# Optimization experiments

Hardware: AMD Instinct MI355X
Metric: run time of the kernel (lower is better)

Reference implementation:

```python
import jax, jax.numpy as jnp
import numpy as np

B = 262144          # batch of sample points
L = 16              # hash levels
T = 1 << 19         # hash table size per level
F = 2               # features per level
BASE_RES = 16
FINEST_RES = 512
DH = 64             # density MLP hidden
DOUT = 16           # density MLP out (density_out dim)
CH = 64             # color MLP hidden
PRIMES = np.array([1, 2654435761, 805459861], dtype=np.uint32)
_b = np.exp((np.log(FINEST_RES) - np.log(BASE_RES)) / (L - 1))
RES = jnp.asarray(np.floor(BASE_RES * _b ** np.arange(L)).astype(np.float32))  # (L,)


def _linear_init(key, fan_in, fan_out):
    kw, kb = jax.random.split(key)
    bound = 1.0 / np.sqrt(fan_in)
    w = jax.random.uniform(kw, (fan_in, fan_out), minval=-bound, maxval=bound)
    b = jax.random.uniform(kb, (fan_out,), minval=-bound, maxval=bound)
    return w, b


def setup_inputs() -> dict:
    key = jax.random.key(0)
    ks = jax.random.split(key, 10)
    coords = jax.random.uniform(ks[0], (B, 3), dtype=jnp.float32)          # in [0,1]
    directions = jax.random.normal(ks[1], (B, 3), dtype=jnp.float32)
    embeddings = jax.random.uniform(ks[2], (L, T, F), minval=-1e-4, maxval=1e-4, dtype=jnp.float32)
    dw1, db1 = _linear_init(ks[3], L * F, DH)
    dw2, db2 = _linear_init(ks[4], DH, DOUT)
    cw1, cb1 = _linear_init(ks[5], 16 + DOUT, CH)
    cw2, cb2 = _linear_init(ks[6], CH, CH)
    cw3, cb3 = _linear_init(ks[7], CH, CH)
    cw4, cb4 = _linear_init(ks[8], CH, 3)
    return dict(coords=coords, directions=directions, embeddings=embeddings,
                dw1=dw1, db1=db1, dw2=dw2, db2=db2,
                cw1=cw1, cb1=cb1, cw2=cw2, cb2=cb2,
                cw3=cw3, cb3=cb3, cw4=cw4, cb4=cb4)


def hash_encode(coords, embeddings):
    # coords: (B,3) in [0,1]; embeddings: (L,T,F)
    pos = coords[:, None, :] * RES[None, :, None]            # (B,L,3)
    p0 = jnp.floor(pos)
    frac = pos - p0                                           # (B,L,3)
    p0 = p0.astype(jnp.uint32)
    corners = jnp.stack([p0, p0 + jnp.uint32(1)], axis=-1)    # (B,L,3,2)
    h_ax = corners * jnp.asarray(PRIMES)[None, None, :, None]  # uint32 wraparound
    hidx = (h_ax[:, :, 0, :, None, None]
            ^ h_ax[:, :, 1, None, :, None]
            ^ h_ax[:, :, 2, None, None, :])                   # (B,L,2,2,2)
    hidx = (hidx & jnp.uint32(T - 1)).reshape(coords.shape[0], L, 8).astype(jnp.int32)
    feats = embeddings[jnp.arange(L)[None, :, None], hidx]    # (B,L,8,F)
    wx = jnp.stack([1.0 - frac[..., 0], frac[..., 0]], -1)    # (B,L,2)
    wy = jnp.stack([1.0 - frac[..., 1], frac[..., 1]], -1)
    wz = jnp.stack([1.0 - frac[..., 2], frac[..., 2]], -1)
    w = (wx[:, :, :, None, None] * wy[:, :, None, :, None] * wz[:, :, None, None, :])
    w = w.reshape(coords.shape[0], L, 8)                      # (B,L,8)
    out = jnp.sum(feats * w[..., None], axis=2)               # (B,L,F)
    return out.reshape(coords.shape[0], L * F)


def sh_encode_deg4(d):
    # d: (B,3) unit directions in [-1,1]; degree-4 real SH basis (16 comps)
    x, y, z = d[:, 0], d[:, 1], d[:, 2]
    xx, yy, zz = x * x, y * y, z * z
    xy, yz, xz = x * y, y * z, x * z
    c = jnp.full_like(x, 0.28209479177387814)
    return jnp.stack([
        c,
        -0.48860251190291987 * y,
        0.48860251190291987 * z,
        -0.48860251190291987 * x,
        1.0925484305920792 * xy,
        -1.0925484305920792 * yz,
        0.94617469575755997 * zz - 0.31539156525251999,
        -1.0925484305920792 * xz,
        0.54627421529603959 * (xx - yy),
        0.59004358992664352 * y * (-3.0 * xx + yy),
        2.8906114426405538 * xy * z,
        0.45704579946446572 * y * (1.0 - 5.0 * zz),
        0.3731763325901154 * z * (5.0 * zz - 3.0),
        0.45704579946446572 * x * (1.0 - 5.0 * zz),
        1.4453057213202769 * z * (xx - yy),
        0.59004358992664352 * x * (xx - 3.0 * yy),
    ], axis=1)


def reference(coords, directions, embeddings, dw1, db1, dw2, db2,
              cw1, cb1, cw2, cb2, cw3, cb3, cw4, cb4):
    # density net: hash encode -> Linear+ReLU -> Linear
    feat = hash_encode(coords, embeddings)                    # (B, L*F)
    h = jax.nn.relu(feat @ dw1 + db1)
    density_out = h @ dw2 + db2                               # (B, DOUT)
    density = jnp.exp(density_out[:, 0])                      # TruncExp fwd = exp
    # color net
    d = directions / jnp.linalg.norm(directions, axis=1, keepdims=True)
    d01 = (d + 1.0) / 2.0                                     # remap as in module
    sh = sh_encode_deg4(d01 * 2.0 - 1.0)                      # encoder maps back to [-1,1]
    inp = jnp.concatenate([sh, density_out], axis=1)          # (B, 32)
    x = jax.nn.relu(inp @ cw1 + cb1)
    x = jax.nn.relu(x @ cw2 + cb2)
    x = jax.nn.relu(x @ cw3 + cb3)
    color = jax.nn.sigmoid(x @ cw4 + cb4)                     # (B, 3)
    return density, color
```

## Files before the change

### kernel.cpp

```cpp
#include <hip/hip_runtime.h>
#include <cmath>

#define NPTS 262144
#define NLVL 16
#define TBL  524288u
#define TMASK 524287u
#define TPB  128
#define NQ   7

typedef __attribute__((ext_vector_type(8))) short short8;
typedef __attribute__((ext_vector_type(4))) float f32x4;

struct ResArr { float r[NLVL]; };
struct QuadInfo { int off[NQ]; int dim[NQ]; };

__device__ __forceinline__ unsigned short f2bf(float f) {
    union { float f; unsigned u; } v; v.f = f;
    unsigned r = v.u + 0x7FFFu + ((v.u >> 16) & 1u);
    return (unsigned short)(r >> 16);
}
__device__ __forceinline__ float blo(unsigned u) {
    union { unsigned v; float f; } x; x.v = u << 16; return x.f;
}
__device__ __forceinline__ float bhi(unsigned u) {
    union { unsigned v; float f; } x; x.v = u & 0xffff0000u; return x.f;
}

#define MFMA(a,b,c) __builtin_amdgcn_mfma_f32_16x16x32_bf16((a),(b),(c),0,0,0)

__global__ __launch_bounds__(256) void wpack_k(
    const float* __restrict__ dw1, const float* __restrict__ db1,
    const float* __restrict__ dw2, const float* __restrict__ db2,
    const float* __restrict__ cw1, const float* __restrict__ cb1,
    const float* __restrict__ cw2, const float* __restrict__ cb2,
    const float* __restrict__ cw3, const float* __restrict__ cb3,
    const float* __restrict__ cw4, const float* __restrict__ cb4,
    unsigned short* __restrict__ wpk, float* __restrict__ bpk)
{
    const int tid  = threadIdx.x;
    const int wid  = tid >> 6;
    const int lane = tid & 63;
    const int m16  = lane & 15;
    const int q    = lane >> 4;

    const unsigned char MAT[28] = {0,0,0,0, 1,1, 2,2,2,2, 3,3,3,3,3,3,3,3, 4,4,4,4,4,4,4,4, 5,5};
    const unsigned char K0 [28] = {0,0,0,0, 0,32, 0,0,0,0, 0,0,0,0,32,32,32,32, 0,0,0,0,32,32,32,32, 0,32};
    const unsigned char N0 [28] = {0,16,32,48, 0,0, 0,16,32,48, 0,16,32,48,0,16,32,48, 0,16,32,48,0,16,32,48, 0,0};

    #pragma unroll
    for (int s = 0; s < 28; ++s) {
        if ((s & 3) == wid) {
            const int mat = MAT[s];
            const float* src = mat==0?dw1 : mat==1?dw2 : mat==2?cw1 : mat==3?cw2 : mat==4?cw3 : cw4;
            const int fan = (mat==1) ? 16 : (mat==5) ? 3 : 64;
            const int k = (int)K0[s] + q*8;
            const int n = (int)N0[s] + m16;
            unsigned short u[8];
            #pragma unroll
            for (int j = 0; j < 8; ++j) {
                float v = 0.f;
                if (mat != 5 || n < 3) v = src[(k+j)*fan + n];
                u[j] = f2bf(v);
            }
            unsigned* w32 = (unsigned*)(wpk + s*512 + lane*8);
            w32[0] = (unsigned)u[0] | ((unsigned)u[1] << 16);
            w32[1] = (unsigned)u[2] | ((unsigned)u[3] << 16);
            w32[2] = (unsigned)u[4] | ((unsigned)u[5] << 16);
            w32[3] = (unsigned)u[6] | ((unsigned)u[7] << 16);
        }
    }
    {
        int t = tid;
        if      (t <  64) bpk[t] = db1[t];
        else if (t <  80) bpk[t] = db2[t-64];
        else if (t < 144) bpk[t] = cb1[t-80];
        else if (t < 208) bpk[t] = cb2[t-144];
    }
    if (tid < 80) {
        int t = tid + 208;
        if (t < 272) bpk[t] = cb3[t-208];
        else         bpk[t] = (t-272 < 3) ? cb4[t-272] : 0.f;
    }
}

__global__ __launch_bounds__(256) void densify_quad_k(
    const float* __restrict__ emb,
    uint4* __restrict__ quad,
    QuadInfo qi)
{
    const int l = blockIdx.y;
    const int t = blockIdx.x * 256 + threadIdx.x;
    const int D = qi.dim[l];
    if (t >= D*D*D) return;
    const unsigned z = (unsigned)t % (unsigned)D;
    const unsigned rem = (unsigned)t / (unsigned)D;
    const unsigned y = rem % (unsigned)D;
    const unsigned x = rem / (unsigned)D;

    const float2* __restrict__ emb2 = (const float2*)emb;
    const unsigned base = (unsigned)l * TBL;
    const unsigned hy0 = y*2654435761u, hy1 = (y+1u)*2654435761u;
    const unsigned hz0 = z*805459861u,  hz1 = (z+1u)*805459861u;

    const float2 a = emb2[base + ((x^hy0^hz0)&TMASK)];
    const float2 b = emb2[base + ((x^hy0^hz1)&TMASK)];
    const float2 c = emb2[base + ((x^hy1^hz0)&TMASK)];
    const float2 d = emb2[base + ((x^hy1^hz1)&TMASK)];

    uint4 q;
    q.x = (unsigned)f2bf(a.x) | ((unsigned)f2bf(a.y) << 16);
    q.y = (unsigned)f2bf(b.x) | ((unsigned)f2bf(b.y) << 16);
    q.z = (unsigned)f2bf(c.x) | ((unsigned)f2bf(c.y) << 16);
    q.w = (unsigned)f2bf(d.x) | ((unsigned)f2bf(d.y) << 16);
    quad[qi.off[l] + t] = q;
}

__global__ __launch_bounds__(256) void hash_encode_k(
    const float* __restrict__ coords,
    const float* __restrict__ emb,
    const uint4* __restrict__ quad,
    unsigned* __restrict__ featws,
    ResArr res, QuadInfo qi)
{
    const int tid = threadIdx.x;
    const int b   = blockIdx.x;
    const int xcd = b & 7;
    const int s   = b >> 3;

    if (s < 1152) {
        int l, p;
        if (s < 1024) {
            l = 7 + xcd;
            p = s * 256 + tid;
        } else {
            l = 15;
            p = xcd * 32768 + (s - 1024) * 256 + tid;
        }

        const float cx = coords[3*p], cy = coords[3*p+1], cz = coords[3*p+2];
        const float r = res.r[l];
        const float px = cx*r, py = cy*r, pz = cz*r;
        const float fpx = floorf(px), fpy = floorf(py), fpz = floorf(pz);
        const float fx = px-fpx, fy = py-fpy, fz = pz-fpz;
        const unsigned ix=(unsigned)fpx, iy=(unsigned)fpy, iz=(unsigned)fpz;
        const unsigned hx0=ix,             hx1=ix+1u;
        const unsigned hy0=iy*2654435761u, hy1=(iy+1u)*2654435761u;
        const unsigned hz0=iz*805459861u,  hz1=(iz+1u)*805459861u;
        const unsigned base = (unsigned)l * TBL;
        const float2* __restrict__ emb2 = (const float2*)emb;

        const float2 f000 = emb2[base + ((hx0^hy0^hz0)&TMASK)];
        const float2 f001 = emb2[base + ((hx0^hy0^hz1)&TMASK)];
        const float2 f010 = emb2[base + ((hx0^hy1^hz0)&TMASK)];
        const float2 f011 = emb2[base + ((hx0^hy1^hz1)&TMASK)];
        const float2 f100 = emb2[base + ((hx1^hy0^hz0)&TMASK)];
        const float2 f101 = emb2[base + ((hx1^hy0^hz1)&TMASK)];
        const float2 f110 = emb2[base + ((hx1^hy1^hz0)&TMASK)];
        const float2 f111 = emb2[base + ((hx1^hy1^hz1)&TMASK)];

        const float wx0=1.f-fx, wy0=1.f-fy, wz0=1.f-fz;
        float o0, o1;
        o0 = wx0*wy0*wz0*f000.x;                 o1 = wx0*wy0*wz0*f000.y;
        o0 = fmaf(wx0*wy0*fz,  f001.x, o0);      o1 = fmaf(wx0*wy0*fz,  f001.y, o1);
        o0 = fmaf(wx0*fy*wz0,  f010.x, o0);      o1 = fmaf(wx0*fy*wz0,  f010.y, o1);
        o0 = fmaf(wx0*fy*fz,   f011.x, o0);      o1 = fmaf(wx0*fy*fz,   f011.y, o1);
        o0 = fmaf(fx*wy0*wz0,  f100.x, o0);      o1 = fmaf(fx*wy0*wz0,  f100.y, o1);
        o0 = fmaf(fx*wy0*fz,   f101.x, o0);      o1 = fmaf(fx*wy0*fz,   f101.y, o1);
        o0 = fmaf(fx*fy*wz0,   f110.x, o0);      o1 = fmaf(fx*fy*wz0,   f110.y, o1);
        o0 = fmaf(fx*fy*fz,    f111.x, o0);      o1 = fmaf(fx*fy*fz,    f111.y, o1);

        featws[(size_t)l * NPTS + p] = (unsigned)f2bf(o0) | ((unsigned)f2bf(o1) << 16);
    } else {
        const int g  = xcd * 224 + (s - 1152);
        const int l  = g >> 8;
        const int c  = g & 255;
        const int D  = qi.dim[l];
        const int DD = D*D;
        const int off = qi.off[l];
        const float r = res.r[l];

        int   pidx[4];
        uint4 qA[4], qB[4];
        float fxa[4], fya[4], fza[4];
        #pragma unroll
        for (int k = 0; k < 4; ++k) {
            const int p = c*1024 + k*256 + tid;
            pidx[k] = p;
            const float cx = coords[3*p], cy = coords[3*p+1], cz = coords[3*p+2];
            const float px = cx*r, py = cy*r, pz = cz*r;
            const float fpx = floorf(px), fpy = floorf(py), fpz = floorf(pz);
            fxa[k] = px-fpx; fya[k] = py-fpy; fza[k] = pz-fpz;
            const int ix=(int)fpx, iy=(int)fpy, iz=(int)fpz;
            const int v0 = off + (ix*D + iy)*D + iz;
            qA[k] = quad[v0];
            qB[k] = quad[v0 + DD];
        }
        #pragma unroll
        for (int k = 0; k < 4; ++k) {
            const float fx = fxa[k], fy = fya[k], fz = fza[k];
            const float wx0=1.f-fx, wy0=1.f-fy, wz0=1.f-fz;
            const float w000=wx0*wy0*wz0, w001=wx0*wy0*fz;
            const float w010=wx0*fy*wz0,  w011=wx0*fy*fz;
            const float w100=fx*wy0*wz0,  w101=fx*wy0*fz;
            const float w110=fx*fy*wz0,   w111=fx*fy*fz;
            float o0, o1;
            o0 = w000*blo(qA[k].x);              o1 = w000*bhi(qA[k].x);
            o0 = fmaf(w001, blo(qA[k].y), o0);   o1 = fmaf(w001, bhi(qA[k].y), o1);
            o0 = fmaf(w010, blo(qA[k].z), o0);   o1 = fmaf(w010, bhi(qA[k].z), o1);
            o0 = fmaf(w011, blo(qA[k].w), o0);   o1 = fmaf(w011, bhi(qA[k].w), o1);
            o0 = fmaf(w100, blo(qB[k].x), o0);   o1 = fmaf(w100, bhi(qB[k].x), o1);
            o0 = fmaf(w101, blo(qB[k].y), o0);   o1 = fmaf(w101, bhi(qB[k].y), o1);
            o0 = fmaf(w110, blo(qB[k].z), o0);   o1 = fmaf(w110, bhi(qB[k].z), o1);
            o0 = fmaf(w111, blo(qB[k].w), o0);   o1 = fmaf(w111, bhi(qB[k].w), o1);
            featws[(size_t)l * NPTS + pidx[k]] =
                (unsigned)f2bf(o0) | ((unsigned)f2bf(o1) << 16);
        }
    }
}

__global__ __launch_bounds__(256, 3) void mlp_mfma_k(
    const unsigned* __restrict__ featws,
    const unsigned short* __restrict__ wpk,
    const float* __restrict__ bpk,
    const float* __restrict__ dirs,
    float* __restrict__ out)
{
    const int tid  = threadIdx.x;
    const int wid  = tid >> 6;
    const int lane = tid & 63;
    const int m16  = lane & 15;
    const int q    = lane >> 4;

    __shared__ __align__(16) unsigned short wlds[28 * 512];
    __shared__ float blds[288];
    __shared__ __align__(16) unsigned short featL[TPB * 40];
    __shared__ __align__(16) unsigned short actL[4 * 16 * 72];

    {
        uint4* dst = (uint4*)wlds;
        const uint4* srcv = (const uint4*)wpk;
        #pragma unroll
        for (int j = 0; j < 7; ++j) dst[j*256 + tid] = srcv[j*256 + tid];
        if (tid < 288) blds[tid] = bpk[tid];
        if (tid < 32)  blds[256 + tid] = bpk[256 + tid];
    }

    const int pbase = blockIdx.x * TPB;
    unsigned* fL32 = (unsigned*)featL;
    #pragma unroll
    for (int j = 0; j < 8; ++j) {
        const int idx  = j*256 + tid;
        const int l    = idx >> 7;
        const int ploc = idx & 127;
        fL32[ploc*20 + l] = featws[(size_t)l * NPTS + pbase + ploc];
    }
    __syncthreads();

    unsigned short* aw = actL + wid*1152;
    const short8* wfr = (const short8*)wlds;

    #pragma unroll
    for (int iter = 0; iter < 2; ++iter) {
        const int tile = wid + 4*iter;
        const int loc0 = tile*16;
        const int p0g  = pbase + loc0;

        short8 a0 = *(const short8*)(featL + (loc0+m16)*40 + q*8);
        f32x4 acc[4];
        #pragma unroll
        for (int nc = 0; nc < 4; ++nc) {
            const float b = blds[nc*16 + m16];
            acc[nc] = (f32x4){b,b,b,b};
            acc[nc] = MFMA(a0, wfr[nc*64 + lane], acc[nc]);
        }
        #pragma unroll
        for (int nc = 0; nc < 4; ++nc)
            #pragma unroll
            for (int r = 0; r < 4; ++r)
                aw[(q*4+r)*72 + nc*16 + m16] = f2bf(fmaxf(acc[nc][r], 0.f));

        short8 ad0 = *(const short8*)(aw + m16*72 + q*8);
        short8 ad1 = *(const short8*)(aw + m16*72 + 32 + q*8);
        f32x4 dob;
        { const float b = blds[64 + m16]; dob = (f32x4){b,b,b,b}; }
        dob = MFMA(ad0, wfr[4*64 + lane], dob);
        dob = MFMA(ad1, wfr[5*64 + lane], dob);

        if (m16 == 0) {
            #pragma unroll
            for (int r = 0; r < 4; ++r) out[p0g + q*4 + r] = expf(dob[r]);
        }

        #pragma unroll
        for (int r = 0; r < 4; ++r)
            aw[(q*4+r)*72 + 16 + m16] = f2bf(dob[r]);
        {
            const int pg = p0g + m16;
            const float dx0 = dirs[3*pg], dy0 = dirs[3*pg+1], dz0 = dirs[3*pg+2];
            const float inv = 1.f / sqrtf(dx0*dx0 + dy0*dy0 + dz0*dz0);
            float x = dx0*inv, y = dy0*inv, z = dz0*inv;
            x = ((x+1.f)*0.5f)*2.f - 1.f;
            y = ((y+1.f)*0.5f)*2.f - 1.f;
            z = ((z+1.f)*0.5f)*2.f - 1.f;
            float s0, s1, s2, s3;
            switch (q) {
            case 0: s0 = 0.28209479177387814f;
                    s1 = -0.48860251190291987f*y;
                    s2 =  0.48860251190291987f*z;
                    s3 = -0.48860251190291987f*x; break;
            case 1: s0 =  1.0925484305920792f*x*y;
                    s1 = -1.0925484305920792f*y*z;
                    s2 =  0.94617469575756f*z*z - 0.31539156525252f;
                    s3 = -1.0925484305920792f*x*z; break;
            case 2: s0 =  0.5462742152960396f*(x*x - y*y);
                    s1 =  0.5900435899266435f*y*(-3.f*x*x + y*y);
                    s2 =  2.890611442640554f*x*y*z;
                    s3 =  0.4570457994644657f*y*(1.f - 5.f*z*z); break;
            default:s0 =  0.3731763325901154f*z*(5.f*z*z - 3.f);
                    s1 =  0.4570457994644657f*x*(1.f - 5.f*z*z);
                    s2 =  1.445305721320277f*z*(x*x - y*y);
                    s3 =  0.5900435899266435f*x*(x*x - 3.f*y*y); break;
            }
            unsigned* ip = (unsigned*)(aw + m16*72 + q*4);
            ip[0] = (unsigned)f2bf(s0) | ((unsigned)f2bf(s1) << 16);
            ip[1] = (unsigned)f2bf(s2) | ((unsigned)f2bf(s3) << 16);
        }

        short8 ac0 = *(const short8*)(aw + m16*72 + q*8);
        #pragma unroll
        for (int nc = 0; nc < 4; ++nc) {
            const float b = blds[80 + nc*16 + m16];
            acc[nc] = (f32x4){b,b,b,b};
            acc[nc] = MFMA(ac0, wfr[(6+nc)*64 + lane], acc[nc]);
        }
        #pragma unroll
        for (int nc = 0; nc < 4; ++nc)
            #pragma unroll
            for (int r = 0; r < 4; ++r)
                aw[(q*4+r)*72 + nc*16 + m16] = f2bf(fmaxf(acc[nc][r], 0.f));

        short8 a20 = *(const short8*)(aw + m16*72 + q*8);
        short8 a21 = *(const short8*)(aw + m16*72 + 32 + q*8);
        #pragma unroll
        for (int nc = 0; nc < 4; ++nc) {
            const float b = blds[144 + nc*16 + m16];
            acc[nc] = (f32x4){b,b,b,b};
            acc[nc] = MFMA(a20, wfr[(10+nc)*64 + lane], acc[nc]);
            acc[nc] = MFMA(a21, wfr[(14+nc)*64 + lane], acc[nc]);
        }
        #pragma unroll
        for (int nc = 0; nc < 4; ++nc)
            #pragma unroll
            for (int r = 0; r < 4; ++r)
                aw[(q*4+r)*72 + nc*16 + m16] = f2bf(fmaxf(acc[nc][r], 0.f));

        short8 a30 = *(const short8*)(aw + m16*72 + q*8);
        short8 a31 = *(const short8*)(aw + m16*72 + 32 + q*8);
        #pragma unroll
        for (int nc = 0; nc < 4; ++nc) {
            const float b = blds[208 + nc*16 + m16];
            acc[nc] = (f32x4){b,b,b,b};
            acc[nc] = MFMA(a30, wfr[(18+nc)*64 + lane], acc[nc]);
            acc[nc] = MFMA(a31, wfr[(22+nc)*64 + lane], acc[nc]);
        }
        #pragma unroll
        for (int nc = 0; nc < 4; ++nc)
            #pragma unroll
            for (int r = 0; r < 4; ++r)
                aw[(q*4+r)*72 + nc*16 + m16] = f2bf(fmaxf(acc[nc][r], 0.f));

        short8 a40 = *(const short8*)(aw + m16*72 + q*8);
        short8 a41 = *(const short8*)(aw + m16*72 + 32 + q*8);
        f32x4 c4;
        { const float b = blds[272 + m16]; c4 = (f32x4){b,b,b,b}; }
        c4 = MFMA(a40, wfr[26*64 + lane], c4);
        c4 = MFMA(a41, wfr[27*64 + lane], c4);
        if (m16 < 3) {
            #pragma unroll
            for (int r = 0; r < 4; ++r)
                out[NPTS + 3*(p0g + q*4 + r) + m16] = 1.f / (1.f + expf(-c4[r]));
        }
    }
}

extern "C" void kernel_launch(void* const* d_in, const int* in_sizes, int n_in,
                              void* d_out, int out_size, void* d_ws, size_t ws_size,
                              hipStream_t stream)
{
    ResArr res;
    const double b = exp((log(512.0) - log(16.0)) / 15.0);
    for (int l = 0; l < NLVL; ++l)
        res.r[l] = (float)floor(16.0 * pow(b, (double)l));

    QuadInfo qi;
    int off = 0, maxn = 0;
    for (int l = 0; l < NQ; ++l) {
        const int D = (int)res.r[l] + 1;
        qi.dim[l] = D;
        qi.off[l] = off;
        off += D*D*D;
        if (D*D*D > maxn) maxn = D*D*D;
    }

    unsigned*       featws = (unsigned*)d_ws;
    uint4*          quad   = (uint4*)((char*)d_ws + (size_t)NLVL * NPTS * 4);
    unsigned short* wpk    = (unsigned short*)((char*)quad + (size_t)off * 16);
    float*          bpk    = (float*)((char*)wpk + 28 * 512 * 2);

    wpack_k<<<1, 256, 0, stream>>>(
        (const float*)d_in[3],  (const float*)d_in[4],
        (const float*)d_in[5],  (const float*)d_in[6],
        (const float*)d_in[7],  (const float*)d_in[8],
        (const float*)d_in[9],  (const float*)d_in[10],
        (const float*)d_in[11], (const float*)d_in[12],
        (const float*)d_in[13], (const float*)d_in[14],
        wpk, bpk);

    densify_quad_k<<<dim3((maxn + 255)/256, NQ), 256, 0, stream>>>(
        (const float*)d_in[2], quad, qi);

    hash_encode_k<<<11008, 256, 0, stream>>>(
        (const float*)d_in[0],
        (const float*)d_in[2],
        quad, featws, res, qi);

    mlp_mfma_k<<<NPTS/TPB, 256, 0, stream>>>(
        featws, wpk, bpk,
        (const float*)d_in[1],
        (float*)d_out);
}
```

Baseline: 254.6 us.

## Store interleaved octet corner data for coarse levels and fuse prep kernels

The densified table for levels 0-5 now stores all eight corners of each cell as two adjacent uint4 entries. A lookup therefore reads 32 contiguous bytes instead of two uint4 loads a full D*D slab apart. Level 6 keeps the old quad layout. The weight-packing kernel and the densify kernel are merged into one launch to drop one kernel launch, at the cost of doubling the dense table storage and densify gather work for the coarse levels.

Result: no change. 259.2 us (+1.8%).

```diff
diff --git a/kernel.cpp b/kernel.cpp
--- a/kernel.cpp
+++ b/kernel.cpp
@@ -25,10 +25,15 @@
 __device__ __forceinline__ float bhi(unsigned u) {
     union { unsigned v; float f; } x; x.v = u & 0xffff0000u; return x.f;
 }
+__device__ __forceinline__ unsigned packbf(float a, float b) {
+    return (unsigned)f2bf(a) | ((unsigned)f2bf(b) << 16);
+}
 
 #define MFMA(a,b,c) __builtin_amdgcn_mfma_f32_16x16x32_bf16((a),(b),(c),0,0,0)
 
-__global__ __launch_bounds__(256) void wpack_k(
+__global__ __launch_bounds__(256) void prep_k(
+    const float* __restrict__ emb,
+    uint4* __restrict__ octq, QuadInfo qi,
     const float* __restrict__ dw1, const float* __restrict__ db1,
     const float* __restrict__ dw2, const float* __restrict__ db2,
     const float* __restrict__ cw1, const float* __restrict__ cb1,
@@ -37,59 +42,56 @@
     const float* __restrict__ cw4, const float* __restrict__ cb4,
     unsigned short* __restrict__ wpk, float* __restrict__ bpk)
 {
-    const int tid  = threadIdx.x;
-    const int wid  = tid >> 6;
-    const int lane = tid & 63;
-    const int m16  = lane & 15;
-    const int q    = lane >> 4;
-
-    const unsigned char MAT[28] = {0,0,0,0, 1,1, 2,2,2,2, 3,3,3,3,3,3,3,3, 4,4,4,4,4,4,4,4, 5,5};
-    const unsigned char K0 [28] = {0,0,0,0, 0,32, 0,0,0,0, 0,0,0,0,32,32,32,32, 0,0,0,0,32,32,32,32, 0,32};
-    const unsigned char N0 [28] = {0,16,32,48, 0,0, 0,16,32,48, 0,16,32,48,0,16,32,48, 0,16,32,48,0,16,32,48, 0,0};
-
-    #pragma unroll
-    for (int s = 0; s < 28; ++s) {
-        if ((s & 3) == wid) {
-            const int mat = MAT[s];
-            const float* src = mat==0?dw1 : mat==1?dw2 : mat==2?cw1 : mat==3?cw2 : mat==4?cw3 : cw4;
-            const int fan = (mat==1) ? 16 : (mat==5) ? 3 : 64;
-            const int k = (int)K0[s] + q*8;
-            const int n = (int)N0[s] + m16;
-            unsigned short u[8];
-            #pragma unroll
-            for (int j = 0; j < 8; ++j) {
-                float v = 0.f;
-                if (mat != 5 || n < 3) v = src[(k+j)*fan + n];
-                u[j] = f2bf(v);
+    const int l = blockIdx.y;
+    const int tid = threadIdx.x;
+
+    if (l == 7) {
+        if (blockIdx.x != 0) return;
+        const int wid  = tid >> 6;
+        const int lane = tid & 63;
+        const int m16  = lane & 15;
+        const int q    = lane >> 4;
+        const unsigned char MAT[28] = {0,0,0,0, 1,1, 2,2,2,2, 3,3,3,3,3,3,3,3, 4,4,4,4,4,4,4,4, 5,5};
+        const unsigned char K0 [28] = {0,0,0,0, 0,32, 0,0,0,0, 0,0,0,0,32,32,32,32, 0,0,0,0,32,32,32,32, 0,32};
+        const unsigned char N0 [28] = {0,16,32,48, 0,0, 0,16,32,48, 0,16,32,48,0,16,32,48, 0,16,32,48,0,16,32,48, 0,0};
+        #pragma unroll
+        for (int s = 0; s < 28; ++s) {
+            if ((s & 3) == wid) {
+                const int mat = MAT[s];
+                const float* src = mat==0?dw1 : mat==1?dw2 : mat==2?cw1 : mat==3?cw2 : mat==4?cw3 : cw4;
+                const int fan = (mat==1) ? 16 : (mat==5) ? 3 : 64;
+                const int k = (int)K0[s] + q*8;
+                const int n = (int)N0[s] + m16;
+                unsigned short u[8];
+                #pragma unroll
+                for (int j = 0; j < 8; ++j) {
+                    float v = 0.f;
+                    if (mat != 5 || n < 3) v = src[(k+j)*fan + n];
+                    u[j] = f2bf(v);
+                }
+                unsigned* w32 = (unsigned*)(wpk + s*512 + lane*8);
+                w32[0] = (unsigned)u[0] | ((unsigned)u[1] << 16);
+                w32[1] = (unsigned)u[2] | ((unsigned)u[3] << 16);
+                w32[2] = (unsigned)u[4] | ((unsigned)u[5] << 16);
+                w32[3] = (unsigned)u[6] | ((unsigned)u[7] << 16);
             }
-            unsigned* w32 = (unsigned*)(wpk + s*512 + lane*8);
-            w32[0] = (unsigned)u[0] | ((unsigned)u[1] << 16);
-            w32[1] = (unsigned)u[2] | ((unsigned)u[3] << 16);
-            w32[2] = (unsigned)u[4] | ((unsigned)u[5] << 16);
-            w32[3] = (unsigned)u[6] | ((unsigned)u[7] << 16);
-        }
-    }
-    {
-        int t = tid;
-        if      (t <  64) bpk[t] = db1[t];
-        else if (t <  80) bpk[t] = db2[t-64];
-        else if (t < 144) bpk[t] = cb1[t-80];
-        else if (t < 208) bpk[t] = cb2[t-144];
-    }
-    if (tid < 80) {
-        int t = tid + 208;
-        if (t < 272) bpk[t] = cb3[t-208];
-        else         bpk[t] = (t-272 < 3) ? cb4[t-272] : 0.f;
-    }
-}
-
-__global__ __launch_bounds__(256) void densify_quad_k(
-    const float* __restrict__ emb,
-    uint4* __restrict__ quad,
-    QuadInfo qi)
-{
-    const int l = blockIdx.y;
-    const int t = blockIdx.x * 256 + threadIdx.x;
+        }
+        {
+            int t = tid;
+            if      (t <  64) bpk[t] = db1[t];
+            else if (t <  80) bpk[t] = db2[t-64];
+            else if (t < 144) bpk[t] = cb1[t-80];
+            else if (t < 208) bpk[t] = cb2[t-144];
+        }
+        if (tid < 80) {
+            int t = tid + 208;
+            if (t < 272) bpk[t] = cb3[t-208];
+            else         bpk[t] = (t-272 < 3) ? cb4[t-272] : 0.f;
+        }
+        return;
+    }
+
+    const int t = blockIdx.x * 256 + tid;
     const int D = qi.dim[l];
     if (t >= D*D*D) return;
     const unsigned z = (unsigned)t % (unsigned)D;
@@ -102,23 +104,38 @@
     const unsigned hy0 = y*2654435761u, hy1 = (y+1u)*2654435761u;
     const unsigned hz0 = z*805459861u,  hz1 = (z+1u)*805459861u;
 
-    const float2 a = emb2[base + ((x^hy0^hz0)&TMASK)];
-    const float2 b = emb2[base + ((x^hy0^hz1)&TMASK)];
-    const float2 c = emb2[base + ((x^hy1^hz0)&TMASK)];
-    const float2 d = emb2[base + ((x^hy1^hz1)&TMASK)];
-
-    uint4 q;
-    q.x = (unsigned)f2bf(a.x) | ((unsigned)f2bf(a.y) << 16);
-    q.y = (unsigned)f2bf(b.x) | ((unsigned)f2bf(b.y) << 16);
-    q.z = (unsigned)f2bf(c.x) | ((unsigned)f2bf(c.y) << 16);
-    q.w = (unsigned)f2bf(d.x) | ((unsigned)f2bf(d.y) << 16);
-    quad[qi.off[l] + t] = q;
+    const float2 a0 = emb2[base + ((x^hy0^hz0)&TMASK)];
+    const float2 b0 = emb2[base + ((x^hy0^hz1)&TMASK)];
+    const float2 c0 = emb2[base + ((x^hy1^hz0)&TMASK)];
+    const float2 d0 = emb2[base + ((x^hy1^hz1)&TMASK)];
+    uint4 qa;
+    qa.x = packbf(a0.x, a0.y);
+    qa.y = packbf(b0.x, b0.y);
+    qa.z = packbf(c0.x, c0.y);
+    qa.w = packbf(d0.x, d0.y);
+
+    if (l < 6) {
+        const unsigned x1 = x + 1u;
+        const float2 a1 = emb2[base + ((x1^hy0^hz0)&TMASK)];
+        const float2 b1 = emb2[base + ((x1^hy0^hz1)&TMASK)];
+        const float2 c1 = emb2[base + ((x1^hy1^hz0)&TMASK)];
+        const float2 d1 = emb2[base + ((x1^hy1^hz1)&TMASK)];
+        uint4 qb;
+        qb.x = packbf(a1.x, a1.y);
+        qb.y = packbf(b1.x, b1.y);
+        qb.z = packbf(c1.x, c1.y);
+        qb.w = packbf(d1.x, d1.y);
+        octq[qi.off[l] + 2*t]     = qa;
+        octq[qi.off[l] + 2*t + 1] = qb;
+    } else {
+        octq[qi.off[6] + t] = qa;
+    }
 }
 
 __global__ __launch_bounds__(256) void hash_encode_k(
     const float* __restrict__ coords,
     const float* __restrict__ emb,
-    const uint4* __restrict__ quad,
+    const uint4* __restrict__ octq,
     unsigned* __restrict__ featws,
     ResArr res, QuadInfo qi)
 {
@@ -169,7 +186,7 @@
         o0 = fmaf(fx*fy*wz0,   f110.x, o0);      o1 = fmaf(fx*fy*wz0,   f110.y, o1);
         o0 = fmaf(fx*fy*fz,    f111.x, o0);      o1 = fmaf(fx*fy*fz,    f111.y, o1);
 
-        featws[(size_t)l * NPTS + p] = (unsigned)f2bf(o0) | ((unsigned)f2bf(o1) << 16);
+        featws[(size_t)l * NPTS + p] = packbf(o0, o1);
     } else {
         const int g  = xcd * 224 + (s - 1152);
         const int l  = g >> 8;
@@ -191,9 +208,14 @@
             const float fpx = floorf(px), fpy = floorf(py), fpz = floorf(pz);
             fxa[k] = px-fpx; fya[k] = py-fpy; fza[k] = pz-fpz;
             const int ix=(int)fpx, iy=(int)fpy, iz=(int)fpz;
-            const int v0 = off + (ix*D + iy)*D + iz;
-            qA[k] = quad[v0];
-            qB[k] = quad[v0 + DD];
+            const int v0 = (ix*D + iy)*D + iz;
+            if (l < 6) {
+                qA[k] = octq[off + 2*v0];
+                qB[k] = octq[off + 2*v0 + 1];
+            } else {
+                qA[k] = octq[off + v0];
+                qB[k] = octq[off + v0 + DD];
+            }
         }
         #pragma unroll
         for (int k = 0; k < 4; ++k) {
@@ -212,8 +234,7 @@
             o0 = fmaf(w101, blo(qB[k].y), o0);   o1 = fmaf(w101, bhi(qB[k].y), o1);
             o0 = fmaf(w110, blo(qB[k].z), o0);   o1 = fmaf(w110, bhi(qB[k].z), o1);
             o0 = fmaf(w111, blo(qB[k].w), o0);   o1 = fmaf(w111, bhi(qB[k].w), o1);
-            featws[(size_t)l * NPTS + pidx[k]] =
-                (unsigned)f2bf(o0) | ((unsigned)f2bf(o1) << 16);
+            featws[(size_t)l * NPTS + pidx[k]] = packbf(o0, o1);
         }
     }
 }
@@ -241,7 +262,7 @@
         const uint4* srcv = (const uint4*)wpk;
         #pragma unroll
         for (int j = 0; j < 7; ++j) dst[j*256 + tid] = srcv[j*256 + tid];
-        if (tid < 288) blds[tid] = bpk[tid];
+        if (tid < 256) blds[tid] = bpk[tid];
         if (tid < 32)  blds[256 + tid] = bpk[256 + tid];
     }
 
@@ -322,8 +343,8 @@
                     s3 =  0.5900435899266435f*x*(x*x - 3.f*y*y); break;
             }
             unsigned* ip = (unsigned*)(aw + m16*72 + q*4);
-            ip[0] = (unsigned)f2bf(s0) | ((unsigned)f2bf(s1) << 16);
-            ip[1] = (unsigned)f2bf(s2) | ((unsigned)f2bf(s3) << 16);
+            ip[0] = packbf(s0, s1);
+            ip[1] = packbf(s2, s3);
         }
 
         short8 ac0 = *(const short8*)(aw + m16*72 + q*8);
@@ -398,16 +419,18 @@
         const int D = (int)res.r[l] + 1;
         qi.dim[l] = D;
         qi.off[l] = off;
-        off += D*D*D;
-        if (D*D*D > maxn) maxn = D*D*D;
+        const int n = D*D*D;
+        off += (l < 6) ? 2*n : n;
+        if (n > maxn) maxn = n;
     }
 
     unsigned*       featws = (unsigned*)d_ws;
-    uint4*          quad   = (uint4*)((char*)d_ws + (size_t)NLVL * NPTS * 4);
-    unsigned short* wpk    = (unsigned short*)((char*)quad + (size_t)off * 16);
+    uint4*          octq   = (uint4*)((char*)d_ws + (size_t)NLVL * NPTS * 4);
+    unsigned short* wpk    = (unsigned short*)((char*)octq + (size_t)off * 16);
     float*          bpk    = (float*)((char*)wpk + 28 * 512 * 2);
 
-    wpack_k<<<1, 256, 0, stream>>>(
+    prep_k<<<dim3((maxn + 255)/256, 8), 256, 0, stream>>>(
+        (const float*)d_in[2], octq, qi,
         (const float*)d_in[3],  (const float*)d_in[4],
         (const float*)d_in[5],  (const float*)d_in[6],
         (const float*)d_in[7],  (const float*)d_in[8],
@@ -416,13 +439,10 @@
         (const float*)d_in[13], (const float*)d_in[14],
         wpk, bpk);
 
-    densify_quad_k<<<dim3((maxn + 255)/256, NQ), 256, 0, stream>>>(
-        (const float*)d_in[2], quad, qi);
-
     hash_encode_k<<<11008, 256, 0, stream>>>(
         (const float*)d_in[0],
         (const float*)d_in[2],
-        quad, featws, res, qi);
+        octq, featws, res, qi);
 
     mlp_mfma_k<<<NPTS/TPB, 256, 0, stream>>>(
         featws, wpk, bpk,
```

## Merge weight-pack and quad-densify kernels; double MLP points per block

Applied to the files above, without the earlier changes.

Folds the weight-packing kernel into the quad-densify kernel as an extra grid row, removing one kernel launch. The MLP kernel now handles 256 points per block instead of 128, with four tile iterations per wave, so the weight copy into LDS is amortized over more points. Launch bounds drop from 3 to 2 blocks per CU to fit the larger feature LDS buffer, which lowers occupancy. The bias copy condition changes from tid<288 to tid<256, which looks like a cleanup of a redundant guard.

Result: no change. 254.2 us (-0.2%).

```diff
diff --git a/kernel.cpp b/kernel.cpp
--- a/kernel.cpp
+++ b/kernel.cpp
@@ -5,7 +5,7 @@
 #define NLVL 16
 #define TBL  524288u
 #define TMASK 524287u
-#define TPB  128
+#define TPB  256
 #define NQ   7
 
 typedef __attribute__((ext_vector_type(8))) short short8;
@@ -25,10 +25,15 @@
 __device__ __forceinline__ float bhi(unsigned u) {
     union { unsigned v; float f; } x; x.v = u & 0xffff0000u; return x.f;
 }
+__device__ __forceinline__ unsigned packbf(float a, float b) {
+    return (unsigned)f2bf(a) | ((unsigned)f2bf(b) << 16);
+}
 
 #define MFMA(a,b,c) __builtin_amdgcn_mfma_f32_16x16x32_bf16((a),(b),(c),0,0,0)
 
-__global__ __launch_bounds__(256) void wpack_k(
+__global__ __launch_bounds__(256) void prep_k(
+    const float* __restrict__ emb,
+    uint4* __restrict__ quad, QuadInfo qi,
     const float* __restrict__ dw1, const float* __restrict__ db1,
     const float* __restrict__ dw2, const float* __restrict__ db2,
     const float* __restrict__ cw1, const float* __restrict__ cb1,
@@ -37,59 +42,56 @@
     const float* __restrict__ cw4, const float* __restrict__ cb4,
     unsigned short* __restrict__ wpk, float* __restrict__ bpk)
 {
-    const int tid  = threadIdx.x;
-    const int wid  = tid >> 6;
-    const int lane = tid & 63;
-    const int m16  = lane & 15;
-    const int q    = lane >> 4;
-
-    const unsigned char MAT[28] = {0,0,0,0, 1,1, 2,2,2,2, 3,3,3,3,3,3,3,3, 4,4,4,4,4,4,4,4, 5,5};
-    const unsigned char K0 [28] = {0,0,0,0, 0,32, 0,0,0,0, 0,0,0,0,32,32,32,32, 0,0,0,0,32,32,32,32, 0,32};
-    const unsigned char N0 [28] = {0,16,32,48, 0,0, 0,16,32,48, 0,16,32,48,0,16,32,48, 0,16,32,48,0,16,32,48, 0,0};
-
-    #pragma unroll
-    for (int s = 0; s < 28; ++s) {
-        if ((s & 3) == wid) {
-            const int mat = MAT[s];
-            const float* src = mat==0?dw1 : mat==1?dw2 : mat==2?cw1 : mat==3?cw2 : mat==4?cw3 : cw4;
-            const int fan = (mat==1) ? 16 : (mat==5) ? 3 : 64;
-            const int k = (int)K0[s] + q*8;
-            const int n = (int)N0[s] + m16;
-            unsigned short u[8];
-            #pragma unroll
-            for (int j = 0; j < 8; ++j) {
-                float v = 0.f;
-                if (mat != 5 || n < 3) v = src[(k+j)*fan + n];
-                u[j] = f2bf(v);
+    const int l = blockIdx.y;
+    const int tid = threadIdx.x;
+
+    if (l == 7) {
+        if (blockIdx.x != 0) return;
+        const int wid  = tid >> 6;
+        const int lane = tid & 63;
+        const int m16  = lane & 15;
+        const int q    = lane >> 4;
+        const unsigned char MAT[28] = {0,0,0,0, 1,1, 2,2,2,2, 3,3,3,3,3,3,3,3, 4,4,4,4,4,4,4,4, 5,5};
+        const unsigned char K0 [28] = {0,0,0,0, 0,32, 0,0,0,0, 0,0,0,0,32,32,32,32, 0,0,0,0,32,32,32,32, 0,32};
+        const unsigned char N0 [28] = {0,16,32,48, 0,0, 0,16,32,48, 0,16,32,48,0,16,32,48, 0,16,32,48,0,16,32,48, 0,0};
+        #pragma unroll
+        for (int s = 0; s < 28; ++s) {
+            if ((s & 3) == wid) {
+                const int mat = MAT[s];
+                const float* src = mat==0?dw1 : mat==1?dw2 : mat==2?cw1 : mat==3?cw2 : mat==4?cw3 : cw4;
+                const int fan = (mat==1) ? 16 : (mat==5) ? 3 : 64;
+                const int k = (int)K0[s] + q*8;
+                const int n = (int)N0[s] + m16;
+                unsigned short u[8];
+                #pragma unroll
+                for (int j = 0; j < 8; ++j) {
+                    float v = 0.f;
+                    if (mat != 5 || n < 3) v = src[(k+j)*fan + n];
+                    u[j] = f2bf(v);
+                }
+                unsigned* w32 = (unsigned*)(wpk + s*512 + lane*8);
+                w32[0] = (unsigned)u[0] | ((unsigned)u[1] << 16);
+                w32[1] = (unsigned)u[2] | ((unsigned)u[3] << 16);
+                w32[2] = (unsigned)u[4] | ((unsigned)u[5] << 16);
+                w32[3] = (unsigned)u[6] | ((unsigned)u[7] << 16);
             }
-            unsigned* w32 = (unsigned*)(wpk + s*512 + lane*8);
-            w32[0] = (unsigned)u[0] | ((unsigned)u[1] << 16);
-            w32[1] = (unsigned)u[2] | ((unsigned)u[3] << 16);
-            w32[2] = (unsigned)u[4] | ((unsigned)u[5] << 16);
-            w32[3] = (unsigned)u[6] | ((unsigned)u[7] << 16);
-        }
-    }
-    {
-        int t = tid;
-        if      (t <  64) bpk[t] = db1[t];
-        else if (t <  80) bpk[t] = db2[t-64];
-        else if (t < 144) bpk[t] = cb1[t-80];
-        else if (t < 208) bpk[t] = cb2[t-144];
-    }
-    if (tid < 80) {
-        int t = tid + 208;
-        if (t < 272) bpk[t] = cb3[t-208];
-        else         bpk[t] = (t-272 < 3) ? cb4[t-272] : 0.f;
-    }
-}
-
-__global__ __launch_bounds__(256) void densify_quad_k(
-    const float* __restrict__ emb,
-    uint4* __restrict__ quad,
-    QuadInfo qi)
-{
-    const int l = blockIdx.y;
-    const int t = blockIdx.x * 256 + threadIdx.x;
+        }
+        {
+            int t = tid;
+            if      (t <  64) bpk[t] = db1[t];
+            else if (t <  80) bpk[t] = db2[t-64];
+            else if (t < 144) bpk[t] = cb1[t-80];
+            else if (t < 208) bpk[t] = cb2[t-144];
+        }
+        if (tid < 80) {
+            int t = tid + 208;
+            if (t < 272) bpk[t] = cb3[t-208];
+            else         bpk[t] = (t-272 < 3) ? cb4[t-272] : 0.f;
+        }
+        return;
+    }
+
+    const int t = blockIdx.x * 256 + tid;
     const int D = qi.dim[l];
     if (t >= D*D*D) return;
     const unsigned z = (unsigned)t % (unsigned)D;
@@ -108,10 +110,10 @@
     const float2 d = emb2[base + ((x^hy1^hz1)&TMASK)];
 
     uint4 q;
-    q.x = (unsigned)f2bf(a.x) | ((unsigned)f2bf(a.y) << 16);
-    q.y = (unsigned)f2bf(b.x) | ((unsigned)f2bf(b.y) << 16);
-    q.z = (unsigned)f2bf(c.x) | ((unsigned)f2bf(c.y) << 16);
-    q.w = (unsigned)f2bf(d.x) | ((unsigned)f2bf(d.y) << 16);
+    q.x = packbf(a.x, a.y);
+    q.y = packbf(b.x, b.y);
+    q.z = packbf(c.x, c.y);
+    q.w = packbf(d.x, d.y);
     quad[qi.off[l] + t] = q;
 }
 
@@ -169,7 +171,7 @@
         o0 = fmaf(fx*fy*wz0,   f110.x, o0);      o1 = fmaf(fx*fy*wz0,   f110.y, o1);
         o0 = fmaf(fx*fy*fz,    f111.x, o0);      o1 = fmaf(fx*fy*fz,    f111.y, o1);
 
-        featws[(size_t)l * NPTS + p] = (unsigned)f2bf(o0) | ((unsigned)f2bf(o1) << 16);
+        featws[(size_t)l * NPTS + p] = packbf(o0, o1);
     } else {
         const int g  = xcd * 224 + (s - 1152);
         const int l  = g >> 8;
@@ -212,13 +214,12 @@
             o0 = fmaf(w101, blo(qB[k].y), o0);   o1 = fmaf(w101, bhi(qB[k].y), o1);
             o0 = fmaf(w110, blo(qB[k].z), o0);   o1 = fmaf(w110, bhi(qB[k].z), o1);
             o0 = fmaf(w111, blo(qB[k].w), o0);   o1 = fmaf(w111, bhi(qB[k].w), o1);
-            featws[(size_t)l * NPTS + pidx[k]] =
-                (unsigned)f2bf(o0) | ((unsigned)f2bf(o1) << 16);
-        }
-    }
-}
-
-__global__ __launch_bounds__(256, 3) void mlp_mfma_k(
+            featws[(size_t)l * NPTS + pidx[k]] = packbf(o0, o1);
+        }
+    }
+}
+
+__global__ __launch_bounds__(256, 2) void mlp_mfma_k(
     const unsigned* __restrict__ featws,
     const unsigned short* __restrict__ wpk,
     const float* __restrict__ bpk,
@@ -241,17 +242,17 @@
         const uint4* srcv = (const uint4*)wpk;
         #pragma unroll
         for (int j = 0; j < 7; ++j) dst[j*256 + tid] = srcv[j*256 + tid];
-        if (tid < 288) blds[tid] = bpk[tid];
+        if (tid < 256) blds[tid] = bpk[tid];
         if (tid < 32)  blds[256 + tid] = bpk[256 + tid];
     }
 
     const int pbase = blockIdx.x * TPB;
     unsigned* fL32 = (unsigned*)featL;
     #pragma unroll
-    for (int j = 0; j < 8; ++j) {
+    for (int j = 0; j < 16; ++j) {
         const int idx  = j*256 + tid;
-        const int l    = idx >> 7;
-        const int ploc = idx & 127;
+        const int l    = idx >> 8;
+        const int ploc = idx & 255;
         fL32[ploc*20 + l] = featws[(size_t)l * NPTS + pbase + ploc];
     }
     __syncthreads();
@@ -260,7 +261,7 @@
     const short8* wfr = (const short8*)wlds;
 
     #pragma unroll
-    for (int iter = 0; iter < 2; ++iter) {
+    for (int iter = 0; iter < 4; ++iter) {
         const int tile = wid + 4*iter;
         const int loc0 = tile*16;
         const int p0g  = pbase + loc0;
@@ -322,8 +323,8 @@
                     s3 =  0.5900435899266435f*x*(x*x - 3.f*y*y); break;
             }
             unsigned* ip = (unsigned*)(aw + m16*72 + q*4);
-            ip[0] = (unsigned)f2bf(s0) | ((unsigned)f2bf(s1) << 16);
-            ip[1] = (unsigned)f2bf(s2) | ((unsigned)f2bf(s3) << 16);
+            ip[0] = packbf(s0, s1);
+            ip[1] = packbf(s2, s3);
         }
 
         short8 ac0 = *(const short8*)(aw + m16*72 + q*8);
@@ -407,7 +408,8 @@
     unsigned short* wpk    = (unsigned short*)((char*)quad + (size_t)off * 16);
     float*          bpk    = (float*)((char*)wpk + 28 * 512 * 2);
 
-    wpack_k<<<1, 256, 0, stream>>>(
+    prep_k<<<dim3((maxn + 255)/256, 8), 256, 0, stream>>>(
+        (const float*)d_in[2], quad, qi,
         (const float*)d_in[3],  (const float*)d_in[4],
         (const float*)d_in[5],  (const float*)d_in[6],
         (const float*)d_in[7],  (const float*)d_in[8],
@@ -416,9 +418,6 @@
         (const float*)d_in[13], (const float*)d_in[14],
         wpk, bpk);
 
-    densify_quad_k<<<dim3((maxn + 255)/256, NQ), 256, 0, stream>>>(
-        (const float*)d_in[2], quad, qi);
-
     hash_encode_k<<<11008, 256, 0, stream>>>(
         (const float*)d_in[0],
         (const float*)d_in[2],
```
